# Kernel optimization log

Hardware: AMD Instinct MI355X
Metric: run time of the kernel (lower is better)

Reference implementation:

```python
import jax, jax.numpy as jnp
import numpy as np

N_EXPERTS = 8
TOP_K = 2
AUX_COEF = 0.01
Z_COEF = 0.001


def setup_inputs() -> dict:
    key = jax.random.key(0)
    ks = jax.random.split(key, 5)
    B, S, D, F, E = 2, 2048, 768, 2048, N_EXPERTS
    std = 0.02
    std_out = std / np.sqrt(2 * 12)  # scale_init_by_depth, n_layers=12
    return {
        "x": jax.random.normal(ks[0], (B, S, D), jnp.float32),
        "router_w": jax.random.normal(ks[1], (D, E), jnp.float32) * std,
        "w1": jax.random.normal(ks[2], (E, D, F), jnp.float32) * std,
        "w2": jax.random.normal(ks[3], (E, F, D), jnp.float32) * std_out,
        "w3": jax.random.normal(ks[4], (E, D, F), jnp.float32) * std,
    }


def reference(x, router_w, w1, w2, w3):
    B, S, D = x.shape
    E = w1.shape[0]
    x_flat = x.reshape(-1, D)                      # [N, D]
    n_tokens = x_flat.shape[0]

    router_logits = x_flat @ router_w               # [N, E]
    probs = jax.nn.softmax(router_logits.astype(jnp.float32), axis=-1)
    topk_w, topk_i = jax.lax.top_k(probs, TOP_K)    # [N, K]
    topk_w = topk_w / jnp.sum(topk_w, axis=-1, keepdims=True)

    # Combine: equivalent to sort/group dispatch + per-expert GEMM + index_add,
    # expressed as a masked per-expert (fixed, small E) dense pass.
    out = jnp.zeros((n_tokens, D), dtype=x.dtype)
    for e in range(E):
        gate = jnp.sum(jnp.where(topk_i == e, topk_w, 0.0), axis=-1)  # [N] f32
        h = jax.nn.silu(x_flat @ w1[e]) * (x_flat @ w3[e])            # [N, F]
        out = out + gate[:, None].astype(x.dtype) * (h @ w2[e])

    # Switch-style load-balancing aux loss + z-loss
    importance = probs.mean(axis=0)                 # [E]
    top1 = topk_i[:, 0]
    load = jnp.zeros((E,), jnp.float32).at[top1].add(1.0) / n_tokens
    aux_loss = E * jnp.sum(importance * load) * AUX_COEF
    z_loss = jnp.mean(router_logits.astype(jnp.float32) ** 2) * Z_COEF

    return out.reshape(B, S, D), aux_loss, z_loss
```

## Files before the change

kernel.cpp:

```cpp
#include <hip/hip_runtime.h>
#include <hip/hip_bf16.h>

constexpr int NT = 4096;
constexpr int DD = 768;
constexpr int FF = 2048;
constexpr int NE = 8;
constexpr int MAXROWS = 9216;
constexpr int MAXMT128 = 72;

constexpr int IDX_CNTA   = 0;
constexpr int IDX_CNTT1  = 8;
constexpr int IDX_CUR    = 16;
constexpr int IDX_IMP    = 24;
constexpr int IDX_ZSUM   = 32;
constexpr int IDX_NTILES = 33;
constexpr int IDX_OFF    = 34;
constexpr int IDX_EXPT   = 48;

constexpr size_t OFF_META   = 0;
constexpr size_t OFF_TKE    = 1024;
constexpr size_t OFF_GATE   = OFF_TKE    + (size_t)NT*2*4;
constexpr size_t OFF_ROWOF  = OFF_GATE   + (size_t)NT*2*4;
constexpr size_t OFF_TOKROW = OFF_ROWOF  + (size_t)NT*2*4;
constexpr size_t OFF_XG     = 136192;
constexpr size_t OFF_W1T    = OFF_XG  + (size_t)MAXROWS*DD*2;
constexpr size_t OFF_W3T    = OFF_W1T + (size_t)NE*FF*DD*2;
constexpr size_t OFF_W2T    = OFF_W3T + (size_t)NE*FF*DD*2;
constexpr size_t OFF_H      = OFF_W2T + (size_t)NE*FF*DD*2;
constexpr size_t OFF_OP     = OFF_H   + (size_t)MAXROWS*FF*2;

typedef float f32x4 __attribute__((ext_vector_type(4)));
typedef __bf16 bf16x8v __attribute__((ext_vector_type(8)));
typedef unsigned short u16x8 __attribute__((ext_vector_type(8)));

__device__ inline unsigned short f2bf_bits(float f) {
  __bf16 h = (__bf16)f;
  return *(unsigned short*)&h;
}
__device__ inline float bf2f(unsigned short u) {
  unsigned v = (unsigned)u << 16;
  return *(float*)&v;
}

__device__ __forceinline__ void glds16(const void* g, void* l) {
  __builtin_amdgcn_global_load_lds(
      (const __attribute__((address_space(1))) unsigned int*)g,
      (__attribute__((address_space(3))) unsigned int*)l, 16, 0, 0);
}

constexpr int RB = 128;
__global__ __launch_bounds__(256) void router_kernel(const float* __restrict__ x,
    const float* __restrict__ rw, int* __restrict__ meta,
    int* __restrict__ tke, float* __restrict__ gateArr) {
  __shared__ float s_imp[NE];
  __shared__ float s_z;
  __shared__ int s_cnt1[NE], s_cnta[NE];
  if (threadIdx.x < NE) { s_imp[threadIdx.x] = 0.f; s_cnt1[threadIdx.x] = 0; s_cnta[threadIdx.x] = 0; }
  if (threadIdx.x == 0) s_z = 0.f;
  __syncthreads();

  const int wave = threadIdx.x >> 6, lane = threadIdx.x & 63;
  float impacc[NE];
  #pragma unroll
  for (int e = 0; e < NE; ++e) impacc[e] = 0.f;
  float zacc = 0.f;

  for (int t = blockIdx.x * 4 + wave; t < NT; t += RB * 4) {
    float acc[NE];
    #pragma unroll
    for (int e = 0; e < NE; ++e) acc[e] = 0.f;
    const float* xr = x + (size_t)t * DD;
    for (int i = lane; i < DD; i += 64) {
      float xv = xr[i];
      const float* r = rw + i * NE;
      #pragma unroll
      for (int e = 0; e < NE; ++e) acc[e] += xv * r[e];
    }
    #pragma unroll
    for (int off = 32; off > 0; off >>= 1) {
      #pragma unroll
      for (int e = 0; e < NE; ++e) acc[e] += __shfl_xor(acc[e], off);
    }
    float mx = acc[0];
    #pragma unroll
    for (int e = 1; e < NE; ++e) mx = fmaxf(mx, acc[e]);
    float p[NE]; float s = 0.f;
    #pragma unroll
    for (int e = 0; e < NE; ++e) { p[e] = __expf(acc[e] - mx); s += p[e]; }
    float inv = 1.f / s;
    #pragma unroll
    for (int e = 0; e < NE; ++e) p[e] *= inv;
    int e0 = 0; float p0 = p[0];
    #pragma unroll
    for (int e = 1; e < NE; ++e) if (p[e] > p0) { p0 = p[e]; e0 = e; }
    int e1 = -1; float p1 = -1.f;
    #pragma unroll
    for (int e = 0; e < NE; ++e) if (e != e0 && p[e] > p1) { p1 = p[e]; e1 = e; }
    if (lane == 0) {
      #pragma unroll
      for (int e = 0; e < NE; ++e) { impacc[e] += p[e]; zacc += acc[e] * acc[e]; }
      atomicAdd(&s_cnt1[e0], 1);
      atomicAdd(&s_cnta[e0], 1);
      atomicAdd(&s_cnta[e1], 1);
      float gs = 1.f / (p0 + p1);
      tke[t*2]   = e0; tke[t*2+1] = e1;
      gateArr[t*2] = p0 * gs; gateArr[t*2+1] = p1 * gs;
    }
  }
  if (lane == 0) {
    #pragma unroll
    for (int e = 0; e < NE; ++e) atomicAdd(&s_imp[e], impacc[e]);
    atomicAdd(&s_z, zacc);
  }
  __syncthreads();
  float* fmeta = (float*)meta;
  if (threadIdx.x < NE) {
    atomicAdd(&fmeta[IDX_IMP + threadIdx.x], s_imp[threadIdx.x]);
    atomicAdd(&meta[IDX_CNTT1 + threadIdx.x], s_cnt1[threadIdx.x]);
    atomicAdd(&meta[IDX_CNTA + threadIdx.x], s_cnta[threadIdx.x]);
  }
  if (threadIdx.x == NE) atomicAdd(&fmeta[IDX_ZSUM], s_z);
}

__global__ __launch_bounds__(128) void scan_kernel(int* __restrict__ meta,
                                                   float* __restrict__ out_tail) {
  __shared__ int s_off[NE + 1];
  __shared__ int s_nt[NE];
  __shared__ float s_aux;
  const int t = threadIdx.x;
  if (t < NE) s_nt[t] = (meta[IDX_CNTA + t] + 127) >> 7;
  __syncthreads();
  if (t == 0) {
    int off = 0;
    for (int e = 0; e < NE; ++e) { s_off[e] = off; off += s_nt[e]; }
    s_off[NE] = off;
  }
  __syncthreads();
  const int ntiles = s_off[NE];
  if (t < NE) meta[IDX_OFF + t] = s_off[t] << 7;
  if (t == NE) { meta[IDX_OFF + NE] = ntiles << 7; meta[IDX_NTILES] = ntiles; }
  if (t < ntiles) {
    int e = 0;
    while (t >= s_off[e + 1]) e++;
    meta[IDX_EXPT + t] = e;
  }
  float* fmeta = (float*)meta;
  float pl = 0.f;
  if (t < NE)
    pl = (fmeta[IDX_IMP + t] / (float)NT) * ((float)meta[IDX_CNTT1 + t] / (float)NT);
  if (t < 64) {
    #pragma unroll
    for (int off = 4; off > 0; off >>= 1) pl += __shfl_xor(pl, off);
    if (t == 0) s_aux = pl;
  }
  __syncthreads();
  if (t == 0) {
    out_tail[0] = (float)NE * s_aux * 0.01f;
    out_tail[1] = fmeta[IDX_ZSUM] / (float)(NT * NE) * 0.001f;
  }
}

__global__ __launch_bounds__(256) void scatter_kernel(const int* __restrict__ tke,
    int* __restrict__ meta, int* __restrict__ rowof, int* __restrict__ tokrow) {
  __shared__ int s_cnt[NE], s_base[NE];
  const int t = blockIdx.x * 256 + threadIdx.x;
  if (threadIdx.x < NE) s_cnt[threadIdx.x] = 0;
  __syncthreads();
  const int e0 = tke[t*2], e1 = tke[t*2 + 1];
  const int l0 = atomicAdd(&s_cnt[e0], 1);
  const int l1 = atomicAdd(&s_cnt[e1], 1);
  __syncthreads();
  if (threadIdx.x < NE)
    s_base[threadIdx.x] = atomicAdd(&meta[IDX_CUR + threadIdx.x], s_cnt[threadIdx.x]);
  __syncthreads();
  const int r0 = meta[IDX_OFF + e0] + s_base[e0] + l0;
  const int r1 = meta[IDX_OFF + e1] + s_base[e1] + l1;
  rowof[t*2]     = r0;
  rowof[t*2 + 1] = r1;
  tokrow[r0] = t;
  tokrow[r1] = t;
}

__global__ __launch_bounds__(192) void gather_kernel(const float* __restrict__ x,
    const int* __restrict__ tokrow, const int* __restrict__ meta,
    __bf16* __restrict__ Xg) {
  const int row = blockIdx.x;
  if (row >= meta[IDX_OFF + NE]) return;
  const int tok = tokrow[row];
  ushort4* dst = (ushort4*)(Xg + (size_t)row * DD);
  const int i = threadIdx.x;
  ushort4 o;
  if (tok >= 0) {
    float4 v = ((const float4*)(x + (size_t)tok * DD))[i];
    o.x = f2bf_bits(v.x); o.y = f2bf_bits(v.y);
    o.z = f2bf_bits(v.z); o.w = f2bf_bits(v.w);
  } else {
    o.x = o.y = o.z = o.w = 0;
  }
  dst[i] = o;
}

constexpr int TS = 68;
__global__ __launch_bounds__(256) void transpose_cvt_all(
    const float* __restrict__ w1, const float* __restrict__ w3,
    const float* __restrict__ w2, __bf16* __restrict__ W1t,
    __bf16* __restrict__ W3t, __bf16* __restrict__ W2t) {
  const int z = blockIdx.z, which = z >> 3, e = z & 7;
  const float* src; __bf16* dst; int R, C, rt, ct;
  if (which == 0)      { src = w1; dst = W1t; R = DD; C = FF; rt = blockIdx.y; ct = blockIdx.x; }
  else if (which == 1) { src = w3; dst = W3t; R = DD; C = FF; rt = blockIdx.y; ct = blockIdx.x; }
  else                 { src = w2; dst = W2t; R = FF; C = DD; rt = blockIdx.x; ct = blockIdx.y; }
  src += (size_t)e * DD * FF; dst += (size_t)e * DD * FF;
  const int r0 = rt * 64, c0 = ct * 64;
  __shared__ __align__(16) __bf16 tile[64 * TS];
  const int t = threadIdx.x;
  #pragma unroll
  for (int i = 0; i < 4; ++i) {
    int idx = t + i * 256; int r = idx >> 4, q = idx & 15;
    float4 v = *(const float4*)&src[(size_t)(r0 + r) * C + c0 + q * 4];
    ushort4 o;
    o.x = f2bf_bits(v.x); o.y = f2bf_bits(v.y);
    o.z = f2bf_bits(v.z); o.w = f2bf_bits(v.w);
    *(ushort4*)&tile[r * TS + q * 4] = o;
  }
  __syncthreads();
  #pragma unroll
  for (int i = 0; i < 2; ++i) {
    int idx = t + i * 256; int c = idx >> 3, seg = idx & 7;
    u16x8 o;
    #pragma unroll
    for (int k = 0; k < 8; ++k)
      o[k] = *(unsigned short*)&tile[(seg * 8 + k) * TS + c];
    *(u16x8*)&dst[(size_t)(c0 + c) * R + r0 + seg * 8] = o;
  }
}

__global__ __launch_bounds__(256) void gemm1_kernel(const __bf16* __restrict__ Xg,
    const __bf16* __restrict__ W1t, const __bf16* __restrict__ W3t,
    __bf16* __restrict__ Hb, const int* __restrict__ meta) {
  const int mt = blockIdx.y;
  if (mt >= meta[IDX_NTILES]) return;
  const int e = meta[IDX_EXPT + mt];
  const int n0 = blockIdx.x * 64;
  const int m0 = mt * 128;
  __shared__ __align__(16) __bf16 As[128*32], B1s[64*32], B3s[64*32];
  const int t = threadIdx.x, wave = t >> 6, lane = t & 63;
  const __bf16* w1e = W1t + (size_t)e * FF * DD;
  const __bf16* w3e = W3t + (size_t)e * FF * DD;
  const f32x4 zero = {0.f, 0.f, 0.f, 0.f};
  f32x4 acc1[2][4], acc3[2][4];
  #pragma unroll
  for (int i = 0; i < 2; ++i)
    #pragma unroll
    for (int j = 0; j < 4; ++j) { acc1[i][j] = zero; acc3[i][j] = zero; }

  const __bf16* gA  = Xg  + (size_t)(m0 + 32*wave + (lane >> 2)) * DD + (lane & 3) * 8;
  const __bf16* gB1 = w1e + (size_t)(n0 + 16*wave + (lane >> 2)) * DD + (lane & 3) * 8;
  const __bf16* gB3 = w3e + (size_t)(n0 + 16*wave + (lane >> 2)) * DD + (lane & 3) * 8;
  __bf16* lA0 = &As [(32*wave     ) * 32];
  __bf16* lA1 = &As [(32*wave + 16) * 32];
  __bf16* lB1 = &B1s[(16*wave     ) * 32];
  __bf16* lB3 = &B3s[(16*wave     ) * 32];

  for (int k0 = 0; k0 < DD; k0 += 32) {
    glds16(gA  + k0,           lA0);
    glds16(gA  + k0 + 16*DD,   lA1);
    glds16(gB1 + k0,           lB1);
    glds16(gB3 + k0,           lB3);
    __syncthreads();
    bf16x8v a[2], b1[4], b3[4];
    #pragma unroll
    for (int i = 0; i < 2; ++i)
      a[i] = *(const bf16x8v*)&As[(32*wave + 16*i + (lane & 15))*32 + (lane >> 4)*8];
    #pragma unroll
    for (int j = 0; j < 4; ++j) {
      b1[j] = *(const bf16x8v*)&B1s[(16*j + (lane & 15))*32 + (lane >> 4)*8];
      b3[j] = *(const bf16x8v*)&B3s[(16*j + (lane & 15))*32 + (lane >> 4)*8];
    }
    #pragma unroll
    for (int i = 0; i < 2; ++i)
      #pragma unroll
      for (int j = 0; j < 4; ++j) {
        acc1[i][j] = __builtin_amdgcn_mfma_f32_16x16x32_bf16(a[i], b1[j], acc1[i][j], 0, 0, 0);
        acc3[i][j] = __builtin_amdgcn_mfma_f32_16x16x32_bf16(a[i], b3[j], acc3[i][j], 0, 0, 0);
      }
    __syncthreads();
  }
  #pragma unroll
  for (int i = 0; i < 2; ++i) {
    const int rowb = m0 + 32*wave + 16*i + (lane >> 4)*4;
    #pragma unroll
    for (int j = 0; j < 4; ++j) {
      const int col = n0 + 16*j + (lane & 15);
      #pragma unroll
      for (int r = 0; r < 4; ++r) {
        float c1 = acc1[i][j][r], c3 = acc3[i][j][r];
        float h = c1 / (1.f + __expf(-c1)) * c3;
        Hb[(size_t)(rowb + r)*FF + col] = (__bf16)h;
      }
    }
  }
}

__global__ __launch_bounds__(256) void gemm2_kernel(const __bf16* __restrict__ Hb,
    const __bf16* __restrict__ W2t, __bf16* __restrict__ OP,
    const int* __restrict__ meta) {
  const int mt = blockIdx.y;
  if (mt >= meta[IDX_NTILES]) return;
  const int e = meta[IDX_EXPT + mt];
  const int n0 = blockIdx.x * 128;
  const int m0 = mt * 128;
  __shared__ __align__(16) __bf16 As[128*32], Bs[128*32];
  const int t = threadIdx.x, wave = t >> 6, lane = t & 63;
  const int wm = wave & 1, wn = wave >> 1;
  const __bf16* w2e = W2t + (size_t)e * DD * FF;
  const f32x4 zero = {0.f, 0.f, 0.f, 0.f};
  f32x4 acc[4][4];
  #pragma unroll
  for (int i = 0; i < 4; ++i)
    #pragma unroll
    for (int j = 0; j < 4; ++j) acc[i][j] = zero;

  const __bf16* gA = Hb  + (size_t)(m0 + 32*wave + (lane >> 2)) * FF + (lane & 3) * 8;
  const __bf16* gB = w2e + (size_t)(n0 + 32*wave + (lane >> 2)) * FF + (lane & 3) * 8;
  __bf16* lA0 = &As[(32*wave     ) * 32];
  __bf16* lA1 = &As[(32*wave + 16) * 32];
  __bf16* lB0 = &Bs[(32*wave     ) * 32];
  __bf16* lB1 = &Bs[(32*wave + 16) * 32];

  for (int k0 = 0; k0 < FF; k0 += 32) {
    glds16(gA + k0,          lA0);
    glds16(gA + k0 + 16*FF,  lA1);
    glds16(gB + k0,          lB0);
    glds16(gB + k0 + 16*FF,  lB1);
    __syncthreads();
    bf16x8v a[4], b[4];
    #pragma unroll
    for (int i = 0; i < 4; ++i) {
      a[i] = *(const bf16x8v*)&As[(64*wm + 16*i + (lane & 15))*32 + (lane >> 4)*8];
      b[i] = *(const bf16x8v*)&Bs[(64*wn + 16*i + (lane & 15))*32 + (lane >> 4)*8];
    }
    #pragma unroll
    for (int i = 0; i < 4; ++i)
      #pragma unroll
      for (int j = 0; j < 4; ++j)
        acc[i][j] = __builtin_amdgcn_mfma_f32_16x16x32_bf16(a[i], b[j], acc[i][j], 0, 0, 0);
    __syncthreads();
  }
  #pragma unroll
  for (int i = 0; i < 4; ++i) {
    const int rowb = m0 + 64*wm + 16*i + (lane >> 4)*4;
    #pragma unroll
    for (int j = 0; j < 4; ++j) {
      const int col = n0 + 64*wn + 16*j + (lane & 15);
      #pragma unroll
      for (int r = 0; r < 4; ++r)
        OP[(size_t)(rowb + r)*DD + col] = (__bf16)acc[i][j][r];
    }
  }
}

__global__ __launch_bounds__(192) void combine_kernel(const __bf16* __restrict__ OP,
    const int* __restrict__ rowof, const float* __restrict__ gateArr,
    float* __restrict__ out) {
  const int t = blockIdx.x;
  const int r0 = rowof[t*2], r1 = rowof[t*2 + 1];
  const float g0 = gateArr[t*2], g1 = gateArr[t*2 + 1];
  const ushort4* p0 = (const ushort4*)(OP + (size_t)r0 * DD);
  const ushort4* p1 = (const ushort4*)(OP + (size_t)r1 * DD);
  const int i = threadIdx.x;
  ushort4 a = p0[i], b = p1[i];
  float4 o;
  o.x = g0 * bf2f(a.x) + g1 * bf2f(b.x);
  o.y = g0 * bf2f(a.y) + g1 * bf2f(b.y);
  o.z = g0 * bf2f(a.z) + g1 * bf2f(b.z);
  o.w = g0 * bf2f(a.w) + g1 * bf2f(b.w);
  ((float4*)(out + (size_t)t * DD))[i] = o;
}

extern "C" void kernel_launch(void* const* d_in, const int* in_sizes, int n_in,
                              void* d_out, int out_size, void* d_ws, size_t ws_size,
                              hipStream_t stream) {
  const float* x  = (const float*)d_in[0];
  const float* rw = (const float*)d_in[1];
  const float* w1 = (const float*)d_in[2];
  const float* w2 = (const float*)d_in[3];
  const float* w3 = (const float*)d_in[4];
  float* out = (float*)d_out;

  char* ws = (char*)d_ws;
  int*    meta   = (int*)(ws + OFF_META);
  int*    tke    = (int*)(ws + OFF_TKE);
  float*  gateA  = (float*)(ws + OFF_GATE);
  int*    rowof  = (int*)(ws + OFF_ROWOF);
  int*    tokrow = (int*)(ws + OFF_TOKROW);
  __bf16* Xg     = (__bf16*)(ws + OFF_XG);
  __bf16* W1t    = (__bf16*)(ws + OFF_W1T);
  __bf16* W3t    = (__bf16*)(ws + OFF_W3T);
  __bf16* W2t    = (__bf16*)(ws + OFF_W2T);
  __bf16* Hb     = (__bf16*)(ws + OFF_H);
  __bf16* OP     = (__bf16*)(ws + OFF_OP);

  hipMemsetAsync(ws + OFF_META, 0, 1024, stream);
  hipMemsetAsync(ws + OFF_TOKROW, 0xFF, (size_t)MAXROWS * 4, stream);

  transpose_cvt_all<<<dim3(32, 12, 24), 256, 0, stream>>>(w1, w3, w2, W1t, W3t, W2t);

  router_kernel<<<RB, 256, 0, stream>>>(x, rw, meta, tke, gateA);
  scan_kernel<<<1, 128, 0, stream>>>(meta, out + (size_t)NT * DD);
  scatter_kernel<<<NT/256, 256, 0, stream>>>(tke, meta, rowof, tokrow);
  gather_kernel<<<MAXROWS, 192, 0, stream>>>(x, tokrow, meta, Xg);

  gemm1_kernel<<<dim3(FF/64, MAXMT128), 256, 0, stream>>>(Xg, W1t, W3t, Hb, meta);
  gemm2_kernel<<<dim3(DD/128, MAXMT128), 256, 0, stream>>>(Hb, W2t, OP, meta);
  combine_kernel<<<NT, 192, 0, stream>>>(OP, rowof, gateA, out);
}
```

Measured before the change: 378.1 us.

## Rewrite gate/up GEMM with 256-row tiles, double-buffered LDS and interleaved W1/W3

The first expert GEMM is rebuilt around 256x(64 w1 + 64 w3) tiles computed by 8 waves, with a 64-wide K step. Global-to-LDS loads go into double-buffered, XOR-swizzled LDS and are interleaved with four MFMA phases using explicit waitcnt, barriers and setprio. Rows of W1 and W3 are interleaved in one B tile so each wave's accumulators hold matching gate/up pairs. The scan kernel now emits a 256-row tile schedule with per-tile row limits. This aims to raise MFMA utilisation and cut redundant loads, at the cost of heavier register and LDS use and of partial tiles doing wasted work.

```diff
diff --git a/kernel.cpp b/kernel.cpp
--- a/kernel.cpp
+++ b/kernel.cpp
@@ -7,6 +7,8 @@
 constexpr int NE = 8;
 constexpr int MAXROWS = 9216;
 constexpr int MAXMT128 = 72;
+constexpr int MAXMT256 = 40;
+constexpr int NKT1 = DD / 64;
 
 constexpr int IDX_CNTA   = 0;
 constexpr int IDX_CNTT1  = 8;
@@ -16,6 +18,10 @@
 constexpr int IDX_NTILES = 33;
 constexpr int IDX_OFF    = 34;
 constexpr int IDX_EXPT   = 48;
+constexpr int IDX_N256   = 120;
+constexpr int IDX_E256   = 128;
+constexpr int IDX_B256   = 168;
+constexpr int IDX_L256   = 208;
 
 constexpr size_t OFF_META   = 0;
 constexpr size_t OFF_TKE    = 1024;
@@ -143,6 +149,21 @@
     int e = 0;
     while (t >= s_off[e + 1]) e++;
     meta[IDX_EXPT + t] = e;
+  }
+  if (t == 0) {
+    int n2t = 0;
+    for (int e = 0; e < NE; ++e) {
+      const int base = s_off[e] << 7;
+      const int lim  = base + (s_nt[e] << 7);
+      const int n2 = (s_nt[e] + 1) >> 1;
+      for (int i = 0; i < n2; ++i) {
+        meta[IDX_E256 + n2t] = e;
+        meta[IDX_B256 + n2t] = base + (i << 8);
+        meta[IDX_L256 + n2t] = lim;
+        ++n2t;
+      }
+    }
+    meta[IDX_N256] = n2t;
   }
   float* fmeta = (float*)meta;
   float pl = 0.f;
@@ -235,68 +256,177 @@
   }
 }
 
-__global__ __launch_bounds__(256) void gemm1_kernel(const __bf16* __restrict__ Xg,
-    const __bf16* __restrict__ W1t, const __bf16* __restrict__ W3t,
-    __bf16* __restrict__ Hb, const int* __restrict__ meta) {
+__global__ __launch_bounds__(512, 2) void gemm1_kernel(
+    const __bf16* __restrict__ Xg, const __bf16* __restrict__ W1t,
+    const __bf16* __restrict__ W3t, __bf16* __restrict__ Hb,
+    const int* __restrict__ meta) {
   const int mt = blockIdx.y;
-  if (mt >= meta[IDX_NTILES]) return;
-  const int e = meta[IDX_EXPT + mt];
-  const int n0 = blockIdx.x * 64;
-  const int m0 = mt * 128;
-  __shared__ __align__(16) __bf16 As[128*32], B1s[64*32], B3s[64*32];
-  const int t = threadIdx.x, wave = t >> 6, lane = t & 63;
-  const __bf16* w1e = W1t + (size_t)e * FF * DD;
-  const __bf16* w3e = W3t + (size_t)e * FF * DD;
+  if (mt >= meta[IDX_N256]) return;
+  const int e      = meta[IDX_E256 + mt];
+  const int m0     = meta[IDX_B256 + mt];
+  const int rowlim = meta[IDX_L256 + mt];
+  const int n0 = blockIdx.x * 128;
+
+  __shared__ __align__(16) __bf16 As[2][256 * 64];
+  __shared__ __align__(16) __bf16 Bs[2][256 * 64];
+
+  const int t = threadIdx.x, lane = t & 63, wid = t >> 6;
+  const int wm = wid >> 2, wn = wid & 3;
+  const int lane15 = lane & 15, g = lane >> 4;
+
+  const __bf16* __restrict__ W1e = W1t + (size_t)e * FF * DD;
+  const __bf16* __restrict__ W3e = W3t + (size_t)e * FF * DD;
+
+  const int aBase = (wm * 128 + lane15) * 64;
+  const int bBase = (wn * 64 + lane15) * 64;
+  const int c0 = ((g    ) ^ (lane & 7)) * 8;
+  const int c1 = ((4 + g) ^ (lane & 7)) * 8;
+
   const f32x4 zero = {0.f, 0.f, 0.f, 0.f};
-  f32x4 acc1[2][4], acc3[2][4];
-  #pragma unroll
-  for (int i = 0; i < 2; ++i)
-    #pragma unroll
-    for (int j = 0; j < 4; ++j) { acc1[i][j] = zero; acc3[i][j] = zero; }
-
-  const __bf16* gA  = Xg  + (size_t)(m0 + 32*wave + (lane >> 2)) * DD + (lane & 3) * 8;
-  const __bf16* gB1 = w1e + (size_t)(n0 + 16*wave + (lane >> 2)) * DD + (lane & 3) * 8;
-  const __bf16* gB3 = w3e + (size_t)(n0 + 16*wave + (lane >> 2)) * DD + (lane & 3) * 8;
-  __bf16* lA0 = &As [(32*wave     ) * 32];
-  __bf16* lA1 = &As [(32*wave + 16) * 32];
-  __bf16* lB1 = &B1s[(16*wave     ) * 32];
-  __bf16* lB3 = &B3s[(16*wave     ) * 32];
-
-  for (int k0 = 0; k0 < DD; k0 += 32) {
-    glds16(gA  + k0,           lA0);
-    glds16(gA  + k0 + 16*DD,   lA1);
-    glds16(gB1 + k0,           lB1);
-    glds16(gB3 + k0,           lB3);
-    __syncthreads();
-    bf16x8v a[2], b1[4], b3[4];
-    #pragma unroll
-    for (int i = 0; i < 2; ++i)
-      a[i] = *(const bf16x8v*)&As[(32*wave + 16*i + (lane & 15))*32 + (lane >> 4)*8];
-    #pragma unroll
-    for (int j = 0; j < 4; ++j) {
-      b1[j] = *(const bf16x8v*)&B1s[(16*j + (lane & 15))*32 + (lane >> 4)*8];
-      b3[j] = *(const bf16x8v*)&B3s[(16*j + (lane & 15))*32 + (lane >> 4)*8];
-    }
-    #pragma unroll
-    for (int i = 0; i < 2; ++i)
-      #pragma unroll
-      for (int j = 0; j < 4; ++j) {
-        acc1[i][j] = __builtin_amdgcn_mfma_f32_16x16x32_bf16(a[i], b1[j], acc1[i][j], 0, 0, 0);
-        acc3[i][j] = __builtin_amdgcn_mfma_f32_16x16x32_bf16(a[i], b3[j], acc3[i][j], 0, 0, 0);
+  f32x4 acc[8][4];
+  #pragma unroll
+  for (int i = 0; i < 8; ++i)
+    #pragma unroll
+    for (int j = 0; j < 4; ++j) acc[i][j] = zero;
+
+  __bf16 *Ac = &As[0][0], *An = &As[1][0];
+  __bf16 *Bc = &Bs[0][0], *Bn = &Bs[1][0];
+
+  auto stage_a = [&](__bf16* dstBuf, int h, int kt) {
+    if (kt >= NKT1) return;
+    #pragma unroll
+    for (int j = 0; j < 2; ++j) {
+      const int o  = j * 512 + t;
+      const int r  = o >> 3;
+      const int cl = (o & 7) ^ (r & 7);
+      int gr = m0 + h * 128 + r;
+      if (gr >= MAXROWS) gr = 0;
+      glds16(Xg + (size_t)gr * DD + kt * 64 + cl * 8,
+             dstBuf + (size_t)(h * 1024 + j * 512 + wid * 64) * 8);
+    }
+  };
+  auto stage_b = [&](__bf16* dstBuf, int h, int kt) {
+    if (kt >= NKT1) return;
+    #pragma unroll
+    for (int j = 0; j < 2; ++j) {
+      const int o  = j * 512 + t;
+      const int r  = o >> 3;
+      const int br = h * 128 + r;
+      const int cl = (o & 7) ^ (r & 7);
+      const __bf16* wsrc = (br & 16) ? W3e : W1e;
+      const int fcol = n0 + ((br >> 5) << 4) + (br & 15);
+      glds16(wsrc + (size_t)fcol * DD + kt * 64 + cl * 8,
+             dstBuf + (size_t)(h * 1024 + j * 512 + wid * 64) * 8);
+    }
+  };
+
+  stage_a(Ac, 0, 0);
+  stage_a(Ac, 1, 0);
+  stage_b(Bc, 0, 0);
+  stage_b(Bc, 1, 0);
+  stage_a(An, 0, 1);
+  stage_a(An, 1, 1);
+  asm volatile("s_waitcnt vmcnt(4)" ::: "memory");
+  __builtin_amdgcn_s_barrier();
+
+  bf16x8v af[8], ag[8], bfr[4], bgr[4];
+
+  for (int k = 0; k < NKT1; ++k) {
+    #pragma unroll
+    for (int i = 0; i < 4; ++i) {
+      af[i*2+0] = *(const bf16x8v*)&Ac[aBase + i*1024 + c0];
+      af[i*2+1] = *(const bf16x8v*)&Ac[aBase + i*1024 + c1];
+    }
+    #pragma unroll
+    for (int j = 0; j < 2; ++j) {
+      bfr[j*2+0] = *(const bf16x8v*)&Bc[bBase + j*1024 + c0];
+      bfr[j*2+1] = *(const bf16x8v*)&Bc[bBase + j*1024 + c1];
+    }
+    stage_b(Bn, 0, k + 1);
+    __builtin_amdgcn_s_barrier();
+    asm volatile("s_waitcnt lgkmcnt(0)" ::: "memory");
+    __builtin_amdgcn_s_setprio(1);
+    #pragma unroll
+    for (int i = 0; i < 4; ++i)
+      #pragma unroll
+      for (int j = 0; j < 2; ++j) {
+        acc[i][j] = __builtin_amdgcn_mfma_f32_16x16x32_bf16(af[i*2+0], bfr[j*2+0], acc[i][j], 0, 0, 0);
+        acc[i][j] = __builtin_amdgcn_mfma_f32_16x16x32_bf16(af[i*2+1], bfr[j*2+1], acc[i][j], 0, 0, 0);
       }
-    __syncthreads();
-  }
-  #pragma unroll
-  for (int i = 0; i < 2; ++i) {
-    const int rowb = m0 + 32*wave + 16*i + (lane >> 4)*4;
-    #pragma unroll
-    for (int j = 0; j < 4; ++j) {
-      const int col = n0 + 16*j + (lane & 15);
+    __builtin_amdgcn_s_setprio(0);
+    __builtin_amdgcn_s_barrier();
+
+    #pragma unroll
+    for (int i = 0; i < 4; ++i) {
+      ag[i*2+0] = *(const bf16x8v*)&Ac[aBase + (4+i)*1024 + c0];
+      ag[i*2+1] = *(const bf16x8v*)&Ac[aBase + (4+i)*1024 + c1];
+    }
+    stage_b(Bn, 1, k + 1);
+    __builtin_amdgcn_s_barrier();
+    asm volatile("s_waitcnt lgkmcnt(0)" ::: "memory");
+    __builtin_amdgcn_s_setprio(1);
+    #pragma unroll
+    for (int i = 0; i < 4; ++i)
+      #pragma unroll
+      for (int j = 0; j < 2; ++j) {
+        acc[4+i][j] = __builtin_amdgcn_mfma_f32_16x16x32_bf16(ag[i*2+0], bfr[j*2+0], acc[4+i][j], 0, 0, 0);
+        acc[4+i][j] = __builtin_amdgcn_mfma_f32_16x16x32_bf16(ag[i*2+1], bfr[j*2+1], acc[4+i][j], 0, 0, 0);
+      }
+    __builtin_amdgcn_s_setprio(0);
+    __builtin_amdgcn_s_barrier();
+
+    #pragma unroll
+    for (int j = 0; j < 2; ++j) {
+      bgr[j*2+0] = *(const bf16x8v*)&Bc[bBase + (2+j)*1024 + c0];
+      bgr[j*2+1] = *(const bf16x8v*)&Bc[bBase + (2+j)*1024 + c1];
+    }
+    stage_a(Ac, 0, k + 2);
+    __builtin_amdgcn_s_barrier();
+    asm volatile("s_waitcnt lgkmcnt(0)" ::: "memory");
+    __builtin_amdgcn_s_setprio(1);
+    #pragma unroll
+    for (int i = 0; i < 4; ++i)
+      #pragma unroll
+      for (int j = 0; j < 2; ++j) {
+        acc[i][2+j] = __builtin_amdgcn_mfma_f32_16x16x32_bf16(af[i*2+0], bgr[j*2+0], acc[i][2+j], 0, 0, 0);
+        acc[i][2+j] = __builtin_amdgcn_mfma_f32_16x16x32_bf16(af[i*2+1], bgr[j*2+1], acc[i][2+j], 0, 0, 0);
+      }
+    __builtin_amdgcn_s_setprio(0);
+    __builtin_amdgcn_s_barrier();
+
+    stage_a(Ac, 1, k + 2);
+    __builtin_amdgcn_s_barrier();
+    __builtin_amdgcn_s_setprio(1);
+    #pragma unroll
+    for (int i = 0; i < 4; ++i)
+      #pragma unroll
+      for (int j = 0; j < 2; ++j) {
+        acc[4+i][2+j] = __builtin_amdgcn_mfma_f32_16x16x32_bf16(ag[i*2+0], bgr[j*2+0], acc[4+i][2+j], 0, 0, 0);
+        acc[4+i][2+j] = __builtin_amdgcn_mfma_f32_16x16x32_bf16(ag[i*2+1], bgr[j*2+1], acc[4+i][2+j], 0, 0, 0);
+      }
+    __builtin_amdgcn_s_setprio(0);
+    if (k < NKT1 - 2) { asm volatile("s_waitcnt vmcnt(4)" ::: "memory"); }
+    else              { asm volatile("s_waitcnt vmcnt(0)" ::: "memory"); }
+    __builtin_amdgcn_s_barrier();
+
+    __bf16* tp;
+    tp = Ac; Ac = An; An = tp;
+    tp = Bc; Bc = Bn; Bn = tp;
+  }
+
+  #pragma unroll
+  for (int i = 0; i < 8; ++i) {
+    const int grow = m0 + wm * 128 + i * 16 + (lane >> 4) * 4;
+    #pragma unroll
+    for (int p = 0; p < 2; ++p) {
+      const int col = n0 + (wn * 2 + p) * 16 + lane15;
+      const f32x4 v1 = acc[i][2*p], v3 = acc[i][2*p + 1];
       #pragma unroll
       for (int r = 0; r < 4; ++r) {
-        float c1 = acc1[i][j][r], c3 = acc3[i][j][r];
-        float h = c1 / (1.f + __expf(-c1)) * c3;
-        Hb[(size_t)(rowb + r)*FF + col] = (__bf16)h;
+        if (grow + r < rowlim) {
+          float h = v1[r] / (1.f + __expf(-v1[r])) * v3[r];
+          Hb[(size_t)(grow + r) * FF + col] = (__bf16)h;
+        }
       }
     }
   }
@@ -411,7 +541,7 @@
   scatter_kernel<<<NT/256, 256, 0, stream>>>(tke, meta, rowof, tokrow);
   gather_kernel<<<MAXROWS, 192, 0, stream>>>(x, tokrow, meta, Xg);
 
-  gemm1_kernel<<<dim3(FF/64, MAXMT128), 256, 0, stream>>>(Xg, W1t, W3t, Hb, meta);
+  gemm1_kernel<<<dim3(FF/128, MAXMT256), 512, 0, stream>>>(Xg, W1t, W3t, Hb, meta);
   gemm2_kernel<<<dim3(DD/128, MAXMT128), 256, 0, stream>>>(Hb, W2t, OP, meta);
   combine_kernel<<<NT, 192, 0, stream>>>(OP, rowof, gateA, out);
 }
```

After: 382.8 us. No clear change (+1.2%).
